# Kernel optimization log

Hardware: AMD Instinct MI355X
Metric: run time of the kernel (lower is better)

Reference implementation:

```python
import jax, jax.numpy as jnp
import numpy as np


def _lstm_scan(x_proj, Wr, units):
    """x_proj: [T, B, 4U] precomputed x@Wk + b. Keras gate order: i, f, g(c), o.
    Returns (all_h [T,B,U], last_h [B,U])."""
    B = x_proj.shape[1]
    h0 = jnp.zeros((B, units), x_proj.dtype)
    c0 = jnp.zeros((B, units), x_proj.dtype)

    def step(carry, xt):
        h, c = carry
        z = xt + h @ Wr                      # [B, 4U]
        i, f, g, o = jnp.split(z, 4, axis=-1)
        i = jax.nn.sigmoid(i)
        f = jax.nn.sigmoid(f)
        g = jnp.tanh(g)
        o = jax.nn.sigmoid(o)
        c = f * c + i * g
        h = o * jnp.tanh(c)
        return (h, c), h

    (h_T, _), hs = jax.lax.scan(step, (h0, c0), x_proj)
    return hs, h_T


def bilstm(x, Wk_f, Wr_f, b_f, Wk_b, Wr_b, b_b):
    units = Wr_f.shape[0]
    # Precompute input projections for all timesteps (one big GEMM per direction)
    xp_f = (x @ Wk_f + b_f).transpose(1, 0, 2)             # [T, B, 4U]
    xp_b = (x[:, ::-1] @ Wk_b + b_b).transpose(1, 0, 2)    # reversed time

    fw_hs, fw_last = _lstm_scan(xp_f, Wr_f, units)         # [T,B,U], [B,U]
    bw_hs, bw_last = _lstm_scan(xp_b, Wr_b, units)

    fw_outputs = fw_hs.transpose(1, 0, 2)                  # [B, T, U]
    # go_backwards outputs are in reverse time order; K.reverse(_, 1) re-aligns
    bw_outputs = bw_hs.transpose(1, 0, 2)[:, ::-1]         # [B, T, U]

    outputs = jnp.concatenate([fw_outputs, bw_outputs], axis=-1)   # [B, T, 2U]
    last_output = jnp.concatenate([fw_last, bw_last], axis=-1)     # [B, 2U]
    return outputs, last_output


def setup_inputs() -> dict:
    key = jax.random.key(0)
    ks = jax.random.split(key, 6)
    B, T, D, U = 32, 512, 256, 256
    s_in = 1.0 / np.sqrt(D)
    s_rec = 1.0 / np.sqrt(U)
    return {
        "x": jax.random.normal(ks[0], (B, T, D), jnp.float32),
        "Wk_f": jax.random.normal(ks[1], (D, 4 * U), jnp.float32) * s_in,
        "Wr_f": jax.random.normal(ks[2], (U, 4 * U), jnp.float32) * s_rec,
        "b_f": jnp.zeros((4 * U,), jnp.float32),
        "Wk_b": jax.random.normal(ks[3], (D, 4 * U), jnp.float32) * s_in,
        "Wr_b": jax.random.normal(ks[4], (U, 4 * U), jnp.float32) * s_rec,
        "b_b": jnp.zeros((4 * U,), jnp.float32),
    }


def reference(x, Wk_f, Wr_f, b_f, Wk_b, Wr_b, b_b):
    return bilstm(x, Wk_f, Wr_f, b_f, Wk_b, Wr_b, b_b)
```

## Files before the change

### kernel.cpp

```cpp
#include <hip/hip_runtime.h>

#define T_STEPS 512
#define BATCH   32
#define DIM     256
#define UNITS   256
#define COLS4U  1024

typedef _Float16 half8  __attribute__((ext_vector_type(8)));
typedef _Float16 half4v __attribute__((ext_vector_type(4)));
typedef float    f32x4  __attribute__((ext_vector_type(4)));
typedef unsigned long long ull;
typedef ull      ull2   __attribute__((ext_vector_type(2)));

__device__ __forceinline__ float fsig(float x){ return 1.0f/(1.0f+__expf(-x)); }
__device__ __forceinline__ float ftanh(float x){
  float xx = fminf(fmaxf(x,-15.f),15.f);
  float e = __expf(2.f*xx);
  return (e-1.f)/(e+1.f);
}

__device__ __forceinline__ int swz(int b, int u){
  int g = u >> 3;
  int s = (g & 7) ^ (b & 7);
  return b*512 + (g>>3)*128 + s*16 + (u & 7)*2;
}

__global__ __launch_bounds__(256, 2) void xproj(
    const float* __restrict__ x,
    const float* __restrict__ Wk_f, const float* __restrict__ b_f,
    const float* __restrict__ Wk_b, const float* __restrict__ b_b,
    _Float16* __restrict__ xph)
{
  const int bx  = blockIdx.x;
  const int dir = bx >> 8;
  const int cg  = (bx >> 5) & 7;
  const int tg  = bx & 31;
  const int tid = threadIdx.x;
  const int w   = tid >> 6;
  const int lane= tid & 63;
  const int l15 = lane & 15;
  const int l4  = lane >> 4;

  const float* Wk = dir ? Wk_b : Wk_f;
  const float* bs = dir ? b_b  : b_f;

  const int col0 = cg*128 + w*32;

  half8 Bf[2][8];
  float bias[2];
#pragma unroll
  for (int nt=0; nt<2; nt++){
    const int col = col0 + nt*16 + l15;
    bias[nt] = bs[col];
#pragma unroll
    for (int kk=0; kk<8; kk++){
      half8 v;
#pragma unroll
      for (int r=0; r<8; r++) v[r] = (_Float16)Wk[(size_t)(kk*32 + l4*8 + r)*COLS4U + col];
      Bf[nt][kk] = v;
    }
  }

  for (int tt=0; tt<16; ++tt){
    const int t   = tg*16 + tt;
    const int tin = dir ? (T_STEPS-1-t) : t;

    half8 Af[2][8];
#pragma unroll
    for (int mt=0; mt<2; mt++){
      const int b = mt*16 + l15;
#pragma unroll
      for (int kk=0; kk<8; kk++){
        const float* xp_ = x + ((size_t)b*T_STEPS + tin)*DIM + kk*32 + l4*8;
        f32x4 u0 = *(const f32x4*)xp_;
        f32x4 u1 = *(const f32x4*)(xp_ + 4);
        half8 v;
        v[0]=(_Float16)u0[0]; v[1]=(_Float16)u0[1]; v[2]=(_Float16)u0[2]; v[3]=(_Float16)u0[3];
        v[4]=(_Float16)u1[0]; v[5]=(_Float16)u1[1]; v[6]=(_Float16)u1[2]; v[7]=(_Float16)u1[3];
        Af[mt][kk] = v;
      }
    }

    f32x4 acc[2][2];
#pragma unroll
    for (int nt=0; nt<2; nt++){
      f32x4 a; a[0]=bias[nt]; a[1]=bias[nt]; a[2]=bias[nt]; a[3]=bias[nt];
      acc[nt][0]=a; acc[nt][1]=a;
    }
#pragma unroll
    for (int kk=0; kk<8; kk++)
#pragma unroll
      for (int nt=0; nt<2; nt++)
#pragma unroll
        for (int mt=0; mt<2; mt++)
          acc[nt][mt] = __builtin_amdgcn_mfma_f32_16x16x32_f16(Af[mt][kk], Bf[nt][kk], acc[nt][mt], 0,0,0);

#pragma unroll
    for (int nt=0; nt<2; nt++){
      const int col = col0 + nt*16 + l15;
#pragma unroll
      for (int mt=0; mt<2; mt++){
        half4v o;
        o[0]=(_Float16)acc[nt][mt][0]; o[1]=(_Float16)acc[nt][mt][1];
        o[2]=(_Float16)acc[nt][mt][2]; o[3]=(_Float16)acc[nt][mt][3];
        *(ull*)(xph + ((size_t)(dir*T_STEPS + t)*COLS4U + col)*BATCH + mt*16 + l4*4)
            = __builtin_bit_cast(ull, o);
      }
    }
  }
}

__global__ __launch_bounds__(512, 2) void bilstm_scan4(
    const float* __restrict__ Wr_f, const float* __restrict__ Wr_b,
    float* __restrict__ out,
    const _Float16* __restrict__ xph,
    unsigned* __restrict__ slices)
{
  const int dir  = blockIdx.x >> 1;
  const int half = blockIdx.x & 1;
  const int tid  = threadIdx.x;
  const int w    = tid >> 6;
  const int lane = tid & 63;
  const int l15  = lane & 15;
  const int l4   = lane >> 4;

  const float* Wr = dir ? Wr_b : Wr_f;

  const int uloc   = w*16 + l15;
  const int unit   = half*128 + uloc;
  const int outcol = dir*256 + unit;

  __shared__ _Float16 hlds[2][BATCH*UNITS];

  half8 Bf[4][8];
#pragma unroll
  for (int q=0; q<4; q++){
    const int col = q*256 + unit;
#pragma unroll
    for (int kk=0; kk<8; kk++){
      half8 v;
#pragma unroll
      for (int r=0; r<8; r++) v[r] = (_Float16)Wr[(size_t)(kk*32 + l4*8 + r)*COLS4U + col];
      Bf[q][kk] = v;
      __builtin_amdgcn_sched_barrier(0);
    }
  }

  {
    half8 z;
#pragma unroll
    for (int e=0; e<8; e++) z[e] = (_Float16)0.f;
    for (int i=tid; i<BATCH*UNITS/8; i+=512) ((half8*)hlds[0])[i] = z;
  }
  __syncthreads();

  const int b_r = tid >> 4;
  const int c0  = (tid & 15) * 8;
  const int pbase = (1-half)*128;

  float cst[8];
#pragma unroll
  for (int i=0;i<8;i++) cst[i]=0.f;
  bool spin_ok = true;

  ull xpv[8];
#pragma unroll
  for (int q=0;q<4;q++)
#pragma unroll
    for (int mt=0;mt<2;mt++)
      xpv[q*2+mt] = *(const ull*)(xph + ((size_t)(dir*T_STEPS + 0)*COLS4U + q*256+unit)*BATCH + mt*16 + l4*4);

  for (int t=0; t<T_STEPS; ++t){
    f32x4 acc[2][4];
#pragma unroll
    for (int q=0;q<4;q++)
#pragma unroll
      for (int mt=0;mt<2;mt++){
        half4v hv = __builtin_bit_cast(half4v, xpv[q*2+mt]);
        f32x4 a; a[0]=(float)hv[0]; a[1]=(float)hv[1]; a[2]=(float)hv[2]; a[3]=(float)hv[3];
        acc[mt][q] = a;
      }

    const char* hpl = (const char*)hlds[t&1];
#pragma unroll
    for (int kk=0; kk<8; kk++){
      const int ul = kk*32 + l4*8;
      half8 a0 = *(const half8*)(hpl + swz(l15,    ul));
      half8 a1 = *(const half8*)(hpl + swz(16+l15, ul));
#pragma unroll
      for (int q=0;q<4;q++){
        acc[0][q] = __builtin_amdgcn_mfma_f32_16x16x32_f16(a0, Bf[q][kk], acc[0][q], 0,0,0);
        acc[1][q] = __builtin_amdgcn_mfma_f32_16x16x32_f16(a1, Bf[q][kk], acc[1][q], 0,0,0);
      }
    }

    const int tout = dir ? (T_STEPS-1-t) : t;
    const int par  = (t+1) & 1;
    unsigned* myslc = slices + ((size_t)(par*4 + dir*2 + half))*4096;
    const unsigned tgt_out = (unsigned)(t+1) & 0xFFFFu;
    char* hnx = (char*)hlds[(t+1)&1];
#pragma unroll
    for (int mt=0; mt<2; mt++){
#pragma unroll
      for (int r=0;r<4;r++){
        const int b = mt*16 + l4*4 + r;
        float iv = fsig (acc[mt][0][r]);
        float fv = fsig (acc[mt][1][r]);
        float gv = ftanh(acc[mt][2][r]);
        float ov = fsig (acc[mt][3][r]);
        float &c = cst[mt*4+r];
        c = fv*c + iv*gv;
        float hv = ov*ftanh(c);
        _Float16 hf = (_Float16)hv;
        if (t+1 < T_STEPS){
          unsigned word = ((unsigned)__builtin_bit_cast(unsigned short, hf) << 16) | tgt_out;
          __hip_atomic_store(&myslc[b*128 + uloc], word,
                             __ATOMIC_RELAXED, __HIP_MEMORY_SCOPE_AGENT);
        }
        *(_Float16*)(hnx + swz(b, unit)) = hf;
        out[((size_t)b*T_STEPS + tout)*(2*UNITS) + outcol] = hv;
        if (t == T_STEPS-1)
          out[(size_t)BATCH*T_STEPS*(2*UNITS) + (size_t)b*(2*UNITS) + outcol] = hv;
      }
    }

    if (t+1 < T_STEPS){
#pragma unroll
      for (int q=0;q<4;q++)
#pragma unroll
        for (int mt=0;mt<2;mt++)
          xpv[q*2+mt] = *(const ull*)(xph + ((size_t)(dir*T_STEPS + (t+1))*COLS4U + q*256+unit)*BATCH + mt*16 + l4*4);

      const ull* src = (const ull*)(slices + ((size_t)(par*4 + dir*2 + (1-half)))*4096
                                    + b_r*128 + c0);
      ull v0,v1,v2,v3;
      if (spin_ok){
        int sp = 0; bool ok;
        do {
          v0 = __hip_atomic_load(&src[0], __ATOMIC_RELAXED, __HIP_MEMORY_SCOPE_AGENT);
          v1 = __hip_atomic_load(&src[1], __ATOMIC_RELAXED, __HIP_MEMORY_SCOPE_AGENT);
          v2 = __hip_atomic_load(&src[2], __ATOMIC_RELAXED, __HIP_MEMORY_SCOPE_AGENT);
          v3 = __hip_atomic_load(&src[3], __ATOMIC_RELAXED, __HIP_MEMORY_SCOPE_AGENT);
          unsigned t0=(unsigned)v0, t1=(unsigned)(v0>>32), t2=(unsigned)v1, t3=(unsigned)(v1>>32);
          unsigned t4=(unsigned)v2, t5=(unsigned)(v2>>32), t6=(unsigned)v3, t7=(unsigned)(v3>>32);
          ok = ((t0&0xFFFF)==tgt_out) & ((t1&0xFFFF)==tgt_out) & ((t2&0xFFFF)==tgt_out)
             & ((t3&0xFFFF)==tgt_out) & ((t4&0xFFFF)==tgt_out) & ((t5&0xFFFF)==tgt_out)
             & ((t6&0xFFFF)==tgt_out) & ((t7&0xFFFF)==tgt_out);
          if (++sp > (1<<20)) { spin_ok = false; break; }
        } while(!ok);
      } else {
        v0 = __hip_atomic_load(&src[0], __ATOMIC_RELAXED, __HIP_MEMORY_SCOPE_AGENT);
        v1 = __hip_atomic_load(&src[1], __ATOMIC_RELAXED, __HIP_MEMORY_SCOPE_AGENT);
        v2 = __hip_atomic_load(&src[2], __ATOMIC_RELAXED, __HIP_MEMORY_SCOPE_AGENT);
        v3 = __hip_atomic_load(&src[3], __ATOMIC_RELAXED, __HIP_MEMORY_SCOPE_AGENT);
      }
      half8 hv;
      {
        unsigned wlo, whi;
        wlo=(unsigned)v0; whi=(unsigned)(v0>>32);
        hv[0]=__builtin_bit_cast(_Float16,(unsigned short)(wlo>>16));
        hv[1]=__builtin_bit_cast(_Float16,(unsigned short)(whi>>16));
        wlo=(unsigned)v1; whi=(unsigned)(v1>>32);
        hv[2]=__builtin_bit_cast(_Float16,(unsigned short)(wlo>>16));
        hv[3]=__builtin_bit_cast(_Float16,(unsigned short)(whi>>16));
        wlo=(unsigned)v2; whi=(unsigned)(v2>>32);
        hv[4]=__builtin_bit_cast(_Float16,(unsigned short)(wlo>>16));
        hv[5]=__builtin_bit_cast(_Float16,(unsigned short)(whi>>16));
        wlo=(unsigned)v3; whi=(unsigned)(v3>>32);
        hv[6]=__builtin_bit_cast(_Float16,(unsigned short)(wlo>>16));
        hv[7]=__builtin_bit_cast(_Float16,(unsigned short)(whi>>16));
      }
      *(half8*)(hnx + swz(b_r, pbase + c0)) = hv;
    }
    __syncthreads();
  }
}

__global__ __launch_bounds__(256,1) void bilstm_mfma(
    const float* __restrict__ x,
    const float* __restrict__ Wk_f, const float* __restrict__ Wr_f, const float* __restrict__ b_f,
    const float* __restrict__ Wk_b, const float* __restrict__ Wr_b, const float* __restrict__ b_b,
    float* __restrict__ out,
    unsigned short* __restrict__ slices,
    unsigned* __restrict__ flags)
{
  const int dir = blockIdx.x >> 2;
  const int g4  = blockIdx.x & 3;
  const int tid = threadIdx.x;
  const int w   = tid >> 6;
  const int lane= tid & 63;
  const int l15 = lane & 15;
  const int l4  = lane >> 4;

  const float* Wk = dir ? Wk_b : Wk_f;
  const float* Wr = dir ? Wr_b : Wr_f;
  const float* bs = dir ? b_b  : b_f;

  const int u0b   = g4*64;
  const int upl   = u0b + w*16 + l15;
  const int outcol= dir*256 + upl;

  __shared__ _Float16 xlds[BATCH*DIM];
  __shared__ _Float16 hlds[2][BATCH*UNITS];

  half8 Bf[4][16];
#pragma unroll
  for (int q=0;q<4;q++){
    const int col = q*256 + upl;
#pragma unroll
    for (int kk=0;kk<16;kk++){
      const float* Ws = (kk<8) ? Wk : Wr;
      const int k0 = (kk&7)*32 + l4*8;
      half8 v;
#pragma unroll
      for (int r=0;r<8;r++) v[r] = (_Float16)Ws[(size_t)(k0+r)*COLS4U + col];
      Bf[q][kk] = v;
      __builtin_amdgcn_sched_barrier(0);
    }
  }

  float bias[4];
#pragma unroll
  for (int q=0;q<4;q++) bias[q] = bs[q*256 + upl];

  {
    half8 z;
#pragma unroll
    for (int e=0;e<8;e++) z[e] = (_Float16)0.f;
    for (int i=tid; i<BATCH*UNITS/8; i+=256) ((half8*)hlds[0])[i] = z;
  }

  const int bx  = tid >> 3;
  const int d0x = (tid & 7) * 32;
  float xr[32];
  {
    const int tin0 = dir ? (T_STEPS-1) : 0;
    const float* xp = x + ((size_t)bx*T_STEPS + tin0)*DIM + d0x;
#pragma unroll
    for (int i=0;i<8;i++){
      f32x4 v = *(const f32x4*)(xp + i*4);
      xr[i*4+0]=v[0]; xr[i*4+1]=v[1]; xr[i*4+2]=v[2]; xr[i*4+3]=v[3];
    }
#pragma unroll
    for (int j=0;j<4;j++){
      half8 hh;
#pragma unroll
      for (int e=0;e<8;e++) hh[e] = (_Float16)xr[j*8+e];
      *(half8*)((char*)xlds + swz(bx, d0x + j*8)) = hh;
    }
  }
  __syncthreads();

  float cst[8];
#pragma unroll
  for (int i=0;i<8;i++) cst[i]=0.f;
  bool spin_ok = true;

  for (int t=0; t<T_STEPS; ++t){
    if (t+1 < T_STEPS){
      const int tin = dir ? (T_STEPS-2-t) : (t+1);
      const float* xp = x + ((size_t)bx*T_STEPS + tin)*DIM + d0x;
#pragma unroll
      for (int i=0;i<8;i++){
        f32x4 v = *(const f32x4*)(xp + i*4);
        xr[i*4+0]=v[0]; xr[i*4+1]=v[1]; xr[i*4+2]=v[2]; xr[i*4+3]=v[3];
      }
    }

    f32x4 acc[2][4];
#pragma unroll
    for (int q=0;q<4;q++){
      f32x4 a; a[0]=bias[q]; a[1]=bias[q]; a[2]=bias[q]; a[3]=bias[q];
      acc[0][q]=a; acc[1][q]=a;
    }
    const char* hpl = (const char*)hlds[t&1];
#pragma unroll
    for (int kk=0;kk<16;kk++){
      const char* pl = (kk<8) ? (const char*)xlds : hpl;
      const int ul = (kk&7)*32 + l4*8;
      half8 a0 = *(const half8*)(pl + swz(l15,      ul));
      half8 a1 = *(const half8*)(pl + swz(16+l15,   ul));
#pragma unroll
      for (int q=0;q<4;q++){
        acc[0][q] = __builtin_amdgcn_mfma_f32_16x16x32_f16(a0, Bf[q][kk], acc[0][q], 0,0,0);
        acc[1][q] = __builtin_amdgcn_mfma_f32_16x16x32_f16(a1, Bf[q][kk], acc[1][q], 0,0,0);
      }
    }

    const int tout = dir ? (T_STEPS-1-t) : t;
    unsigned short* slc = slices + (((size_t)((t+1)&1))*8 + dir*4 + g4)*2048;
    char* hnx = (char*)hlds[(t+1)&1];
#pragma unroll
    for (int mt=0; mt<2; mt++){
#pragma unroll
      for (int r=0;r<4;r++){
        const int b = mt*16 + l4*4 + r;
        float iv = fsig (acc[mt][0][r]);
        float fv = fsig (acc[mt][1][r]);
        float gv = ftanh(acc[mt][2][r]);
        float ov = fsig (acc[mt][3][r]);
        float &c = cst[mt*4+r];
        c = fv*c + iv*gv;
        float hval = ov*ftanh(c);
        out[((size_t)b*T_STEPS + tout)*(2*UNITS) + outcol] = hval;
        if (t == T_STEPS-1)
          out[(size_t)BATCH*T_STEPS*(2*UNITS) + (size_t)b*(2*UNITS) + outcol] = hval;
        _Float16 hf = (_Float16)hval;
        *(_Float16*)(hnx + swz(b, upl)) = hf;
        if (t+1 < T_STEPS)
          __hip_atomic_store(&slc[b*64 + (w*16+l15)],
                             __builtin_bit_cast(unsigned short, hf),
                             __ATOMIC_RELAXED, __HIP_MEMORY_SCOPE_AGENT);
      }
    }
    __syncthreads();

    if (t+1 < T_STEPS){
      if (tid == 192)
        __hip_atomic_store(&flags[(dir*4+g4)*32], (unsigned)(t+1),
                           __ATOMIC_RELAXED, __HIP_MEMORY_SCOPE_AGENT);
#pragma unroll
      for (int j=0;j<4;j++){
        half8 hh;
#pragma unroll
        for (int e=0;e<8;e++) hh[e] = (_Float16)xr[j*8+e];
        *(half8*)((char*)xlds + swz(bx, d0x + j*8)) = hh;
      }
      if (w < 3){
        const int p = w + (w >= g4);
        const unsigned target = (unsigned)(t+1);
        if (spin_ok){
          int sp = 0;
          while (__hip_atomic_load(&flags[(dir*4+p)*32],
                                   __ATOMIC_RELAXED, __HIP_MEMORY_SCOPE_AGENT) < target){
            if (++sp > (1<<22)) { spin_ok = false; break; }
          }
        }
        const ull* src = (const ull*)(slices + (((size_t)((t+1)&1))*8 + dir*4 + p)*2048);
        const int bsl = lane >> 1;
        const int u00 = (lane & 1) * 32;
#pragma unroll
        for (int j=0;j<4;j++){
          ull v0 = __hip_atomic_load(&src[lane*8 + 2*j  ], __ATOMIC_RELAXED, __HIP_MEMORY_SCOPE_AGENT);
          ull v1 = __hip_atomic_load(&src[lane*8 + 2*j+1], __ATOMIC_RELAXED, __HIP_MEMORY_SCOPE_AGENT);
          ull2 vv; vv[0]=v0; vv[1]=v1;
          *(ull2*)(hnx + swz(bsl, p*64 + u00 + j*8)) = vv;
        }
      }
      __syncthreads();
    }
  }
}

extern "C" void kernel_launch(void* const* d_in, const int* in_sizes, int n_in,
                              void* d_out, int out_size, void* d_ws, size_t ws_size,
                              hipStream_t stream) {
  const float* x    = (const float*)d_in[0];
  const float* Wk_f = (const float*)d_in[1];
  const float* Wr_f = (const float*)d_in[2];
  const float* b_f  = (const float*)d_in[3];
  const float* Wk_b = (const float*)d_in[4];
  const float* Wr_b = (const float*)d_in[5];
  const float* b_b  = (const float*)d_in[6];
  float* out = (float*)d_out;

  const size_t XPH = (size_t)2*T_STEPS*COLS4U*BATCH*sizeof(_Float16);
  const size_t SL  = (size_t)2*2*2*BATCH*128*sizeof(unsigned);

  if (ws_size >= XPH + SL) {
    _Float16* xph    = (_Float16*)d_ws;
    unsigned* slices = (unsigned*)((char*)d_ws + XPH);
    xproj<<<512, 256, 0, stream>>>(x, Wk_f, b_f, Wk_b, b_b, xph);
    bilstm_scan4<<<4, 512, 0, stream>>>(Wr_f, Wr_b, out, xph, slices);
  } else {
    unsigned short* slices = (unsigned short*)d_ws;
    unsigned* flags = (unsigned*)((char*)d_ws + 65536);
    hipMemsetAsync((char*)d_ws + 65536, 0, 1024, stream);
    bilstm_mfma<<<8, 256, 0, stream>>>(x, Wk_f, Wr_f, b_f, Wk_b, Wr_b, b_b,
                                       out, slices, flags);
  }
}
```

Before: 2.842 ms.

## Run each LSTM direction on one workgroup, splitting Wr across registers, LDS and L2

Replaces the two-workgroups-per-direction scan, which traded half of h through global memory with spin-waited atomics, with one 512-thread workgroup per direction that computes all 1024 gate columns. The recurrent weights are repacked once into an fp16 swizzled layout by a new kernel. Three k-tiles stay in registers, two sit in LDS, and three are streamed from global/L2 on every step with some software prefetch. This removes the cross-CU handshake latency each step. In exchange, each CU does twice the MFMA work per step and reloads weights from cache every step.

Result: slower. 8.672 ms (+205.1%).

```diff
diff --git a/kernel.cpp b/kernel.cpp
--- a/kernel.cpp
+++ b/kernel.cpp
@@ -14,15 +14,32 @@
 
 __device__ __forceinline__ float fsig(float x){ return 1.0f/(1.0f+__expf(-x)); }
 __device__ __forceinline__ float ftanh(float x){
-  float xx = fminf(fmaxf(x,-15.f),15.f);
-  float e = __expf(2.f*xx);
+  float xx=fminf(fmaxf(x,-15.f),15.f);
+  float e=__expf(2.f*xx);
   return (e-1.f)/(e+1.f);
 }
-
-__device__ __forceinline__ int swz(int b, int u){
-  int g = u >> 3;
-  int s = (g & 7) ^ (b & 7);
-  return b*512 + (g>>3)*128 + s*16 + (u & 7)*2;
+__device__ __forceinline__ int swz(int b,int u){
+  int g=u>>3; int s=(g&7)^(b&7);
+  return b*512 + (g>>3)*128 + s*16 + (u&7)*2;
+}
+__device__ __forceinline__ int gran(int col,int q){
+  return ((col<<2) | q) ^ ((col>>1)&7);
+}
+
+__global__ __launch_bounds__(256) void repack(
+    const float* __restrict__ Wr_f, const float* __restrict__ Wr_b,
+    _Float16* __restrict__ rp)
+{
+  const int idx = blockIdx.x*256 + threadIdx.x;
+  const int q   = idx & 3;
+  const int col = (idx>>2) & 1023;
+  const int kt  = (idx>>12) & 7;
+  const int dir = idx >> 15;
+  const float* Wr = dir ? Wr_b : Wr_f;
+  half8 v;
+#pragma unroll
+  for (int r=0;r<8;r++) v[r] = (_Float16)Wr[(size_t)(kt*32 + q*8 + r)*COLS4U + col];
+  *(half8*)(rp + ((size_t)((dir*8 + kt)*4096 + gran(col,q)) << 3)) = v;
 }
 
 __global__ __launch_bounds__(256, 2) void xproj(
@@ -110,167 +127,155 @@
   }
 }
 
-__global__ __launch_bounds__(512, 2) void bilstm_scan4(
-    const float* __restrict__ Wr_f, const float* __restrict__ Wr_b,
+__global__ __launch_bounds__(512, 2) void bilstm_1cu(
+    const _Float16* __restrict__ rp,
     float* __restrict__ out,
-    const _Float16* __restrict__ xph,
-    unsigned* __restrict__ slices)
+    const _Float16* __restrict__ xph)
 {
-  const int dir  = blockIdx.x >> 1;
-  const int half = blockIdx.x & 1;
-  const int tid  = threadIdx.x;
-  const int w    = tid >> 6;
-  const int lane = tid & 63;
-  const int l15  = lane & 15;
-  const int l4   = lane >> 4;
-
-  const float* Wr = dir ? Wr_b : Wr_f;
-
-  const int uloc   = w*16 + l15;
-  const int unit   = half*128 + uloc;
-  const int outcol = dir*256 + unit;
-
-  __shared__ _Float16 hlds[2][BATCH*UNITS];
-
-  half8 Bf[4][8];
-#pragma unroll
-  for (int q=0; q<4; q++){
-    const int col = q*256 + unit;
-#pragma unroll
-    for (int kk=0; kk<8; kk++){
-      half8 v;
-#pragma unroll
-      for (int r=0; r<8; r++) v[r] = (_Float16)Wr[(size_t)(kk*32 + l4*8 + r)*COLS4U + col];
-      Bf[q][kk] = v;
-      __builtin_amdgcn_sched_barrier(0);
-    }
-  }
-
-  {
-    half8 z;
-#pragma unroll
-    for (int e=0; e<8; e++) z[e] = (_Float16)0.f;
-    for (int i=tid; i<BATCH*UNITS/8; i+=512) ((half8*)hlds[0])[i] = z;
-  }
+  const int dir = (int)blockIdx.x;
+  const int tid = threadIdx.x;
+  const int w   = tid >> 6;
+  const int lane= tid & 63;
+  const int l15 = lane & 15;
+  const int l4  = lane >> 4;
+
+  __shared__ _Float16 stash[2*4096*8];
+  __shared__ _Float16 hpl[BATCH*UNITS];
+
+  int col[8];
+#pragma unroll
+  for (int nt=0; nt<8; nt++)
+    col[nt] = (nt>>1)*256 + w*32 + (nt&1)*16 + l15;
+
+  const _Float16* rpd = rp + ((size_t)dir*8*4096 << 3);
+
+  half8 Bf[8][3];
+#pragma unroll
+  for (int nt=0; nt<8; nt++)
+#pragma unroll
+    for (int kt=0; kt<3; kt++)
+      Bf[nt][kt] = *(const half8*)(rpd + ((size_t)(kt*4096 + gran(col[nt],l4)) << 3));
+
+  for (int i=tid; i<8192; i+=512)
+    *(ull2*)(stash + ((size_t)i<<3)) = *(const ull2*)(rpd + ((size_t)(3*4096 + i) << 3));
+
+  for (int i=tid; i<2048; i+=512) ((ull*)hpl)[i] = 0ull;
   __syncthreads();
 
-  const int b_r = tid >> 4;
-  const int c0  = (tid & 15) * 8;
-  const int pbase = (1-half)*128;
-
-  float cst[8];
-#pragma unroll
-  for (int i=0;i<8;i++) cst[i]=0.f;
-  bool spin_ok = true;
-
-  ull xpv[8];
-#pragma unroll
-  for (int q=0;q<4;q++)
-#pragma unroll
-    for (int mt=0;mt<2;mt++)
-      xpv[q*2+mt] = *(const ull*)(xph + ((size_t)(dir*T_STEPS + 0)*COLS4U + q*256+unit)*BATCH + mt*16 + l4*4);
+  float cst[16];
+#pragma unroll
+  for (int i=0;i<16;i++) cst[i]=0.f;
+
+  const _Float16* xpt = xph + (size_t)dir*T_STEPS*COLS4U*BATCH;
 
   for (int t=0; t<T_STEPS; ++t){
-    f32x4 acc[2][4];
-#pragma unroll
-    for (int q=0;q<4;q++)
-#pragma unroll
-      for (int mt=0;mt<2;mt++){
-        half4v hv = __builtin_bit_cast(half4v, xpv[q*2+mt]);
+    f32x4 acc[2][8];
+#pragma unroll
+    for (int mt=0; mt<2; mt++)
+#pragma unroll
+      for (int nt=0; nt<8; nt++){
+        ull xv = *(const ull*)(xpt + (size_t)t*32768 + col[nt]*32 + mt*16 + l4*4);
+        half4v hv = __builtin_bit_cast(half4v, xv);
         f32x4 a; a[0]=(float)hv[0]; a[1]=(float)hv[1]; a[2]=(float)hv[2]; a[3]=(float)hv[3];
-        acc[mt][q] = a;
-      }
-
-    const char* hpl = (const char*)hlds[t&1];
-#pragma unroll
-    for (int kk=0; kk<8; kk++){
-      const int ul = kk*32 + l4*8;
-      half8 a0 = *(const half8*)(hpl + swz(l15,    ul));
-      half8 a1 = *(const half8*)(hpl + swz(16+l15, ul));
-#pragma unroll
-      for (int q=0;q<4;q++){
-        acc[0][q] = __builtin_amdgcn_mfma_f32_16x16x32_f16(a0, Bf[q][kk], acc[0][q], 0,0,0);
-        acc[1][q] = __builtin_amdgcn_mfma_f32_16x16x32_f16(a1, Bf[q][kk], acc[1][q], 0,0,0);
-      }
-    }
+        acc[mt][nt] = a;
+      }
+
+    half8 SA[8], SB[8];
+#pragma unroll
+    for (int nt=0; nt<8; nt++)
+      SA[nt] = *(const half8*)(rpd + ((size_t)(5*4096 + gran(col[nt],l4)) << 3));
+
+#pragma unroll
+    for (int kt=0; kt<3; kt++){
+      const int ul = kt*32 + l4*8;
+      half8 a0 = *(const half8*)((const char*)hpl + swz(l15,    ul));
+      half8 a1 = *(const half8*)((const char*)hpl + swz(16+l15, ul));
+#pragma unroll
+      for (int nt=0; nt<8; nt++){
+        acc[0][nt] = __builtin_amdgcn_mfma_f32_16x16x32_f16(a0, Bf[nt][kt], acc[0][nt], 0,0,0);
+        acc[1][nt] = __builtin_amdgcn_mfma_f32_16x16x32_f16(a1, Bf[nt][kt], acc[1][nt], 0,0,0);
+      }
+    }
+
+#pragma unroll
+    for (int ks=0; ks<2; ks++){
+      const int kt = 3 + ks;
+      const int ul = kt*32 + l4*8;
+      half8 a0 = *(const half8*)((const char*)hpl + swz(l15,    ul));
+      half8 a1 = *(const half8*)((const char*)hpl + swz(16+l15, ul));
+#pragma unroll
+      for (int nt=0; nt<8; nt++){
+        half8 bs = *(const half8*)(stash + ((size_t)(ks*4096 + gran(col[nt],l4)) << 3));
+        acc[0][nt] = __builtin_amdgcn_mfma_f32_16x16x32_f16(a0, bs, acc[0][nt], 0,0,0);
+        acc[1][nt] = __builtin_amdgcn_mfma_f32_16x16x32_f16(a1, bs, acc[1][nt], 0,0,0);
+      }
+    }
+
+    {
+#pragma unroll
+      for (int nt=0; nt<8; nt++)
+        SB[nt] = *(const half8*)(rpd + ((size_t)(6*4096 + gran(col[nt],l4)) << 3));
+      {
+        const int ul = 5*32 + l4*8;
+        half8 a0 = *(const half8*)((const char*)hpl + swz(l15,    ul));
+        half8 a1 = *(const half8*)((const char*)hpl + swz(16+l15, ul));
+#pragma unroll
+        for (int nt=0; nt<8; nt++){
+          acc[0][nt] = __builtin_amdgcn_mfma_f32_16x16x32_f16(a0, SA[nt], acc[0][nt], 0,0,0);
+          acc[1][nt] = __builtin_amdgcn_mfma_f32_16x16x32_f16(a1, SA[nt], acc[1][nt], 0,0,0);
+        }
+      }
+#pragma unroll
+      for (int nt=0; nt<8; nt++)
+        SA[nt] = *(const half8*)(rpd + ((size_t)(7*4096 + gran(col[nt],l4)) << 3));
+      {
+        const int ul = 6*32 + l4*8;
+        half8 a0 = *(const half8*)((const char*)hpl + swz(l15,    ul));
+        half8 a1 = *(const half8*)((const char*)hpl + swz(16+l15, ul));
+#pragma unroll
+        for (int nt=0; nt<8; nt++){
+          acc[0][nt] = __builtin_amdgcn_mfma_f32_16x16x32_f16(a0, SB[nt], acc[0][nt], 0,0,0);
+          acc[1][nt] = __builtin_amdgcn_mfma_f32_16x16x32_f16(a1, SB[nt], acc[1][nt], 0,0,0);
+        }
+      }
+      {
+        const int ul = 7*32 + l4*8;
+        half8 a0 = *(const half8*)((const char*)hpl + swz(l15,    ul));
+        half8 a1 = *(const half8*)((const char*)hpl + swz(16+l15, ul));
+#pragma unroll
+        for (int nt=0; nt<8; nt++){
+          acc[0][nt] = __builtin_amdgcn_mfma_f32_16x16x32_f16(a0, SA[nt], acc[0][nt], 0,0,0);
+          acc[1][nt] = __builtin_amdgcn_mfma_f32_16x16x32_f16(a1, SA[nt], acc[1][nt], 0,0,0);
+        }
+      }
+    }
+
+    __syncthreads();
 
     const int tout = dir ? (T_STEPS-1-t) : t;
-    const int par  = (t+1) & 1;
-    unsigned* myslc = slices + ((size_t)(par*4 + dir*2 + half))*4096;
-    const unsigned tgt_out = (unsigned)(t+1) & 0xFFFFu;
-    char* hnx = (char*)hlds[(t+1)&1];
-#pragma unroll
-    for (int mt=0; mt<2; mt++){
-#pragma unroll
-      for (int r=0;r<4;r++){
-        const int b = mt*16 + l4*4 + r;
-        float iv = fsig (acc[mt][0][r]);
-        float fv = fsig (acc[mt][1][r]);
-        float gv = ftanh(acc[mt][2][r]);
-        float ov = fsig (acc[mt][3][r]);
-        float &c = cst[mt*4+r];
-        c = fv*c + iv*gv;
-        float hv = ov*ftanh(c);
-        _Float16 hf = (_Float16)hv;
-        if (t+1 < T_STEPS){
-          unsigned word = ((unsigned)__builtin_bit_cast(unsigned short, hf) << 16) | tgt_out;
-          __hip_atomic_store(&myslc[b*128 + uloc], word,
-                             __ATOMIC_RELAXED, __HIP_MEMORY_SCOPE_AGENT);
-        }
-        *(_Float16*)(hnx + swz(b, unit)) = hf;
-        out[((size_t)b*T_STEPS + tout)*(2*UNITS) + outcol] = hv;
-        if (t == T_STEPS-1)
-          out[(size_t)BATCH*T_STEPS*(2*UNITS) + (size_t)b*(2*UNITS) + outcol] = hv;
-      }
-    }
-
-    if (t+1 < T_STEPS){
-#pragma unroll
-      for (int q=0;q<4;q++)
-#pragma unroll
-        for (int mt=0;mt<2;mt++)
-          xpv[q*2+mt] = *(const ull*)(xph + ((size_t)(dir*T_STEPS + (t+1))*COLS4U + q*256+unit)*BATCH + mt*16 + l4*4);
-
-      const ull* src = (const ull*)(slices + ((size_t)(par*4 + dir*2 + (1-half)))*4096
-                                    + b_r*128 + c0);
-      ull v0,v1,v2,v3;
-      if (spin_ok){
-        int sp = 0; bool ok;
-        do {
-          v0 = __hip_atomic_load(&src[0], __ATOMIC_RELAXED, __HIP_MEMORY_SCOPE_AGENT);
-          v1 = __hip_atomic_load(&src[1], __ATOMIC_RELAXED, __HIP_MEMORY_SCOPE_AGENT);
-          v2 = __hip_atomic_load(&src[2], __ATOMIC_RELAXED, __HIP_MEMORY_SCOPE_AGENT);
-          v3 = __hip_atomic_load(&src[3], __ATOMIC_RELAXED, __HIP_MEMORY_SCOPE_AGENT);
-          unsigned t0=(unsigned)v0, t1=(unsigned)(v0>>32), t2=(unsigned)v1, t3=(unsigned)(v1>>32);
-          unsigned t4=(unsigned)v2, t5=(unsigned)(v2>>32), t6=(unsigned)v3, t7=(unsigned)(v3>>32);
-          ok = ((t0&0xFFFF)==tgt_out) & ((t1&0xFFFF)==tgt_out) & ((t2&0xFFFF)==tgt_out)
-             & ((t3&0xFFFF)==tgt_out) & ((t4&0xFFFF)==tgt_out) & ((t5&0xFFFF)==tgt_out)
-             & ((t6&0xFFFF)==tgt_out) & ((t7&0xFFFF)==tgt_out);
-          if (++sp > (1<<20)) { spin_ok = false; break; }
-        } while(!ok);
-      } else {
-        v0 = __hip_atomic_load(&src[0], __ATOMIC_RELAXED, __HIP_MEMORY_SCOPE_AGENT);
-        v1 = __hip_atomic_load(&src[1], __ATOMIC_RELAXED, __HIP_MEMORY_SCOPE_AGENT);
-        v2 = __hip_atomic_load(&src[2], __ATOMIC_RELAXED, __HIP_MEMORY_SCOPE_AGENT);
-        v3 = __hip_atomic_load(&src[3], __ATOMIC_RELAXED, __HIP_MEMORY_SCOPE_AGENT);
-      }
-      half8 hv;
-      {
-        unsigned wlo, whi;
-        wlo=(unsigned)v0; whi=(unsigned)(v0>>32);
-        hv[0]=__builtin_bit_cast(_Float16,(unsigned short)(wlo>>16));
-        hv[1]=__builtin_bit_cast(_Float16,(unsigned short)(whi>>16));
-        wlo=(unsigned)v1; whi=(unsigned)(v1>>32);
-        hv[2]=__builtin_bit_cast(_Float16,(unsigned short)(wlo>>16));
-        hv[3]=__builtin_bit_cast(_Float16,(unsigned short)(whi>>16));
-        wlo=(unsigned)v2; whi=(unsigned)(v2>>32);
-        hv[4]=__builtin_bit_cast(_Float16,(unsigned short)(wlo>>16));
-        hv[5]=__builtin_bit_cast(_Float16,(unsigned short)(whi>>16));
-        wlo=(unsigned)v3; whi=(unsigned)(v3>>32);
-        hv[6]=__builtin_bit_cast(_Float16,(unsigned short)(wlo>>16));
-        hv[7]=__builtin_bit_cast(_Float16,(unsigned short)(whi>>16));
-      }
-      *(half8*)(hnx + swz(b_r, pbase + c0)) = hv;
+#pragma unroll
+    for (int un=0; un<2; un++){
+      const int unit = w*32 + un*16 + l15;
+      const int oc   = dir*256 + unit;
+#pragma unroll
+      for (int mt=0; mt<2; mt++){
+#pragma unroll
+        for (int r=0; r<4; r++){
+          const int b = mt*16 + l4*4 + r;
+          float iv = fsig (acc[mt][0+un][r]);
+          float fv = fsig (acc[mt][2+un][r]);
+          float gv = ftanh(acc[mt][4+un][r]);
+          float ov = fsig (acc[mt][6+un][r]);
+          float &c = cst[(mt*2+un)*4 + r];
+          c = fv*c + iv*gv;
+          float hv = ov*ftanh(c);
+          if (t+1 < T_STEPS)
+            *(_Float16*)((char*)hpl + swz(b, unit)) = (_Float16)hv;
+          out[((size_t)b*T_STEPS + tout)*(2*UNITS) + oc] = hv;
+          if (t == T_STEPS-1)
+            out[(size_t)BATCH*T_STEPS*(2*UNITS) + (size_t)b*(2*UNITS) + oc] = hv;
+        }
+      }
     }
     __syncthreads();
   }
@@ -373,10 +378,10 @@
       f32x4 a; a[0]=bias[q]; a[1]=bias[q]; a[2]=bias[q]; a[3]=bias[q];
       acc[0][q]=a; acc[1][q]=a;
     }
-    const char* hpl = (const char*)hlds[t&1];
+    const char* hpl2 = (const char*)hlds[t&1];
 #pragma unroll
     for (int kk=0;kk<16;kk++){
-      const char* pl = (kk<8) ? (const char*)xlds : hpl;
+      const char* pl = (kk<8) ? (const char*)xlds : hpl2;
       const int ul = (kk&7)*32 + l4*8;
       half8 a0 = *(const half8*)(pl + swz(l15,      ul));
       half8 a1 = *(const half8*)(pl + swz(16+l15,   ul));
@@ -465,13 +470,14 @@
   float* out = (float*)d_out;
 
   const size_t XPH = (size_t)2*T_STEPS*COLS4U*BATCH*sizeof(_Float16);
-  const size_t SL  = (size_t)2*2*2*BATCH*128*sizeof(unsigned);
-
-  if (ws_size >= XPH + SL) {
-    _Float16* xph    = (_Float16*)d_ws;
-    unsigned* slices = (unsigned*)((char*)d_ws + XPH);
+  const size_t RPB = (size_t)2*8*4096*8*sizeof(_Float16);
+
+  if (ws_size >= XPH + RPB) {
+    _Float16* xph = (_Float16*)d_ws;
+    _Float16* rp  = (_Float16*)((char*)d_ws + XPH);
+    repack<<<256, 256, 0, stream>>>(Wr_f, Wr_b, rp);
     xproj<<<512, 256, 0, stream>>>(x, Wk_f, b_f, Wk_b, b_b, xph);
-    bilstm_scan4<<<4, 512, 0, stream>>>(Wr_f, Wr_b, out, xph, slices);
+    bilstm_1cu<<<2, 512, 0, stream>>>(rp, out, xph);
   } else {
     unsigned short* slices = (unsigned short*)d_ws;
     unsigned* flags = (unsigned*)((char*)d_ws + 65536);
```
